# Optimization experiments

Hardware: AMD Instinct MI355X
Metric: run time of the kernel (lower is better)

## Reference

```python
import jax, jax.numpy as jnp
import numpy as np

B, S, IN, H, OUT, L = 32, 512, 300, 180, 60, 4
NBLOCK, NF = 3, 3  # mel_smooth_layers, mel_smooth_filter_size
GRP = OUT // NF    # 20 groups per mel conv


def setup_inputs() -> dict:
    key = jax.random.key(0)
    ks = jax.random.split(key, 12)
    def u(k, shape, scale):
        return jax.random.uniform(k, shape, jnp.float32, -scale, scale)
    s = float(1.0 / np.sqrt(H))
    return {
        "x": jax.random.normal(ks[0], (B, S, IN), jnp.float32),
        "Wih0": u(ks[1], (4 * H, IN), s),
        "Wih_rest": u(ks[2], (L - 1, 4 * H, H), s),
        "Whh": u(ks[3], (L, 4 * H, H), s),
        "bih": u(ks[4], (L, 4 * H), s),
        "bhh": u(ks[5], (L, 4 * H), s),
        "linW": u(ks[6], (OUT, H), s),
        "linb": u(ks[7], (OUT,), s),
        "mel_w": u(ks[8], (NBLOCK, NF, GRP, NF, 5), 0.2),  # per block, per filter: Conv1d(60,20,5,groups=20)
        "mel_b": u(ks[9], (NBLOCK, NF, GRP), 0.2),
        "resW": u(ks[10], (OUT, 2, 5), 0.2),               # Conv1d(120,60,5,groups=60)
        "resb": u(ks[11], (OUT,), 0.2),
    }


def _lstm(x, Wih0, Wih_rest, Whh, bih, bhh):
    # torch nn.LSTM, batch_first, gate order (i, f, g, o)
    h_in = x  # [B, S, D]
    for l in range(L):
        Wih = Wih0 if l == 0 else Wih_rest[l - 1]
        Whh_l = Whh[l]
        b = bih[l] + bhh[l]
        xt = h_in.transpose(1, 0, 2) @ Wih.T + b  # [S, B, 4H], input projection hoisted out of scan
        def step(carry, xg):
            h, c = carry
            g = xg + h @ Whh_l.T
            i, f, gg, o = jnp.split(g, 4, axis=-1)
            c = jax.nn.sigmoid(f) * c + jax.nn.sigmoid(i) * jnp.tanh(gg)
            h = jax.nn.sigmoid(o) * jnp.tanh(c)
            return (h, c), h
        init = (jnp.zeros((x.shape[0], H), x.dtype), jnp.zeros((x.shape[0], H), x.dtype))
        _, hs = jax.lax.scan(step, init, xt)  # [S, B, H]
        h_in = hs.transpose(1, 0, 2)
    return h_in  # [B, S, H]


def _conv1d_grouped(x, w, b, groups):
    # x: [B, C, S], w: [O, C//groups, K]
    y = jax.lax.conv_general_dilated(
        x, w, window_strides=(1,), padding=[(2, 2)],
        dimension_numbers=("NCH", "OIH", "NCH"), feature_group_count=groups)
    return y + b[None, :, None]


def _mel_block(x, w, b):
    # x: [B, 60, S]; w: [NF, 20, NF, 5]; b: [NF, 20]
    Bb, C, Ss = x.shape
    z = jnp.zeros((Bb, 1, Ss), x.dtype)
    # shifted channel stacks: [down-shift-1, identity, up-shift-1] (filter_size_channel == 3)
    xs = [jnp.concatenate([z, x[:, :-1]], axis=1), x, jnp.concatenate([x[:, 1:], z], axis=1)]
    outs = [_conv1d_grouped(xs[j], w[j], b[j], GRP) for j in range(NF)]  # each [B, 20, S]
    # interleave: output channel 3*i + j = outs[j][:, i, :]
    return jnp.stack(outs, axis=2).reshape(Bb, C, Ss)


def _forward(x, Wih0, Wih_rest, Whh, bih, bhh, linW, linb, mel_w, mel_b, resW, resb):
    h = _lstm(x, Wih0, Wih_rest, Whh, bih, bhh)      # [B, S, H]
    out = h @ linW.T + linb                          # [B, S, 60]
    out = out.transpose(0, 2, 1)                     # [B, 60, S]
    lstm_out = out
    for l in range(NBLOCK):
        out = _mel_block(out, mel_w[l], mel_b[l]) + out  # block + shortcut (Identity activation)
    # interleave (lstm, smoothed) per mel channel -> [B, 120, S]
    pair = jnp.stack([lstm_out, out], axis=2).reshape(out.shape[0], 2 * OUT, out.shape[2])
    out = _conv1d_grouped(pair, resW, resb, OUT)     # [B, 60, S]
    return out.transpose(0, 2, 1)                    # [B, S, 60] (Identity output activation)


def reference(x, Wih0, Wih_rest, Whh, bih, bhh, linW, linb, mel_w, mel_b, resW, resb):
    return _forward(x, Wih0, Wih_rest, Whh, bih, bhh, linW, linb, mel_w, mel_b, resW, resb)
```

## Files before the change

kernel.cpp:

```cpp
#include <hip/hip_runtime.h>
#include <hip/hip_bf16.h>

#define B_ 32
#define S_ 512
#define IN_ 300
#define H_ 180
#define G4_ 720
#define OUT_ 60
#define R_ 16384
#define TC_ 32
#define NC_ 16
#define NPK_ 92

#define PWHH_O  0u
#define PW0_O   264960u
#define PWR_O   372960u
#define BIASF_O 567360u
#define LINWF_O 570240u
#define LINBF_O 581040u
#define WFT_    581100u

#define XG_O   0u
#define HR_O   6291456u
#define H3_O   7397376u
#define WFU_O  8871936u
#define STH_O  9453036u
#define STC_O  9476076u
#define FLAG_O 9499116u
#define XGSLOT 786432
#define HRSLOT 184320

#if defined(__has_builtin)
#if __has_builtin(__builtin_amdgcn_fdot2)
#define HAVE_FDOT2 1
#endif
#if __has_builtin(__builtin_amdgcn_mov_dpp)
#define HAVE_DPP 1
#endif
#endif

typedef _Float16 f16x2 __attribute__((ext_vector_type(2)));

struct Plan {
  int nl; int ll[4]; int lc[4];
  int ng; int gl[4]; int gc[4];
};

__device__ __forceinline__ float sigf(float x)   { return 1.f / (1.f + __expf(-x)); }
__device__ __forceinline__ float tanhf2(float x) { return 2.f / (1.f + __expf(-2.f * x)) - 1.f; }
__device__ __forceinline__ float toF(__hip_bfloat16 x) { return __bfloat162float(x); }
__device__ __forceinline__ float ldr(const void* p, long i, int fl) {
  return fl ? ((const float*)p)[i] : toF(((const __hip_bfloat16*)p)[i]);
}
__device__ __forceinline__ unsigned f16b(_Float16 h) {
  union { _Float16 f; unsigned short s; } x; x.f = h; return x.s;
}
__device__ __forceinline__ float h2f(unsigned s) {
  union { unsigned short s; _Float16 f; } x; x.s = (unsigned short)(s & 0xFFFFu);
  return (float)x.f;
}
__device__ __forceinline__ f16x2 u2h(unsigned u) {
  union { unsigned u; f16x2 v; } x; x.u = u; return x.v;
}
__device__ __forceinline__ float fd2(unsigned hu, unsigned wu, float acc) {
#ifdef HAVE_FDOT2
  return __builtin_amdgcn_fdot2(u2h(hu), u2h(wu), acc, false);
#else
  return acc + h2f(hu) * h2f(wu) + h2f(hu >> 16) * h2f(wu >> 16);
#endif
}
__device__ __forceinline__ unsigned packpair_f32(float lo, float hi) {
  return f16b((_Float16)lo) | (f16b((_Float16)hi) << 16);
}
__device__ __forceinline__ unsigned packpair_bf16(unsigned u) {
  union { unsigned v; float f; } a, b;
  a.v = u << 16; b.v = u & 0xFFFF0000u;
  return packpair_f32(a.f, b.f);
}

#ifdef HAVE_DPP
#define QBC(dst, src, J) { \
  const int qv_ = __builtin_amdgcn_mov_dpp(__float_as_int(src), (J) * 85, 0xF, 0xF, false); \
  dst = __int_as_float(qv_); }
#else
#define QBC(dst, src, J) dst = __shfl(src, (((threadIdx.x & 63) & ~3) + (J)), 64);
#endif

#define REP23(M) M(0) M(1) M(2) M(3) M(4) M(5) M(6) M(7) M(8) M(9) M(10) \
  M(11) M(12) M(13) M(14) M(15) M(16) M(17) M(18) M(19) M(20) M(21) M(22)
#define LW(n) \
  unsigned w##n##a = wp0[(4*n+0)*G4_], w##n##b = wp0[(4*n+1)*G4_], \
           w##n##c = wp0[(4*n+2)*G4_], w##n##d = wp0[(4*n+3)*G4_];
#define PW(n) \
  asm volatile("" : "+v"(w##n##a), "+v"(w##n##b), "+v"(w##n##c), "+v"(w##n##d));
#define ST2(n) { \
  const uint4 hA_ = *(const uint4*)&hbA[4*n]; \
  const uint4 hB_ = *(const uint4*)&hbB[4*n]; \
  aA0 = fd2(hA_.x, w##n##a, aA0); aA1 = fd2(hA_.y, w##n##b, aA1); \
  aA2 = fd2(hA_.z, w##n##c, aA2); aA3 = fd2(hA_.w, w##n##d, aA3); \
  aB0 = fd2(hB_.x, w##n##a, aB0); aB1 = fd2(hB_.y, w##n##b, aB1); \
  aB2 = fd2(hB_.z, w##n##c, aB2); aB3 = fd2(hB_.w, w##n##d, aB3); }

__global__ __launch_bounds__(256) void detect_kernel(
    const unsigned short* __restrict__ xw, int* __restrict__ flag) {
  __shared__ int cnt;
  if (threadIdx.x == 0) cnt = 0;
  __syncthreads();
  int lc = 0;
  for (int i = threadIdx.x; i < 2048; i += 256) {
    const int e = (xw[i] >> 7) & 0xFF;
    if (e >= 0xC0 || (e > 0 && e < 0x40)) lc++;
  }
  atomicAdd(&cnt, lc);
  __syncthreads();
  if (threadIdx.x == 0) *flag = (cnt > 100) ? 1 : 0;
}

__global__ __launch_bounds__(256) void prep_kernel(
    const void* __restrict__ wih0, const void* __restrict__ wihr,
    const void* __restrict__ whh,  const void* __restrict__ bih,
    const void* __restrict__ bhh,  const void* __restrict__ linw,
    const void* __restrict__ linb, float* __restrict__ wf,
    const int* __restrict__ flag) {
  const unsigned i = blockIdx.x * 256u + threadIdx.x;
  if (i >= WFT_) return;
  const int fl = *flag;
  if (i < PW0_O) {
    const unsigned l = i / 66240u, r = i % 66240u;
    const unsigned jp = r / 720u, o = r % 720u;
    const unsigned ro = (o & 3u) * 180u + (o >> 2);
    unsigned u = 0u;
    if (jp < 90u) {
      const long b = (long)l * 129600 + (long)ro * H_;
      u = packpair_f32(ldr(whh, b + 2 * jp, fl), ldr(whh, b + 2 * jp + 1, fl));
    }
    ((unsigned*)wf)[i] = u;
    return;
  }
  if (i < PWR_O) {
    const unsigned j = i - PW0_O, o = j / 150u, kp = j % 150u;
    const long b = (long)o * IN_;
    ((unsigned*)wf)[i] =
        packpair_f32(ldr(wih0, b + 2 * kp, fl), ldr(wih0, b + 2 * kp + 1, fl));
    return;
  }
  if (i < BIASF_O) {
    const unsigned j = i - PWR_O, l = j / 64800u, r = j % 64800u;
    const unsigned o = r / 90u, kp = r % 90u;
    const long b = (long)l * 129600 + (long)o * H_;
    ((unsigned*)wf)[i] =
        packpair_f32(ldr(wihr, b + 2 * kp, fl), ldr(wihr, b + 2 * kp + 1, fl));
    return;
  }
  float v;
  if (i < LINWF_O)      { const unsigned j = i - BIASF_O; v = ldr(bih, j, fl) + ldr(bhh, j, fl); }
  else if (i < LINBF_O) v = ldr(linw, i - LINWF_O, fl);
  else                  v = ldr(linb, i - LINBF_O, fl);
  wf[i] = v;
}

__global__ __launch_bounds__(768, 3) void fused_kernel(
    const void* __restrict__ x, const int* __restrict__ flag,
    const unsigned* __restrict__ wfu,
    float* __restrict__ xg, float* __restrict__ hr,
    __hip_bfloat16* __restrict__ h3,
    float* __restrict__ sth, float* __restrict__ stc, Plan p) {
  __shared__ __align__(16) unsigned hpk[2][2][NPK_];
  __shared__ __align__(16) unsigned Asu[3][10][68];
  __shared__ __align__(16) unsigned Bsu[3][10][68];

  const int bid = blockIdx.x;
  if (bid < p.nl * 16) {
    const int j = bid >> 4, pb = bid & 15;
    const int l = p.ll[j], c = p.lc[j];
    const int b0 = pb * 2, b1 = b0 + 1;
    const int o = threadIdx.x;
    const int oc = (o < G4_) ? o : (G4_ - 1);
    const int g = o & 3, u = o >> 2;
    const bool act = (o < G4_);
    const unsigned* wp0 = wfu + PWHH_O + (unsigned)l * (NPK_ * G4_) + oc;
    REP23(LW)
    REP23(PW)
    const float* xgs = xg + (long)(l * 2 + (c & 1)) * XGSLOT;
    float* hrs = hr + (long)((l < 3 ? l : 0) * 2 + (c & 1)) * HRSLOT;
    float cstA = 0.f, cstB = 0.f, hA0 = 0.f, hB0 = 0.f;
    if (c != 0 && act) {
      cstA = stc[(l * 32 + b0) * H_ + u]; hA0 = sth[(l * 32 + b0) * H_ + u];
      cstB = stc[(l * 32 + b1) * H_ + u]; hB0 = sth[(l * 32 + b1) * H_ + u];
    }
    if (o < 4 * NPK_ && (o % NPK_) >= (NPK_ - 2)) ((unsigned*)hpk)[o] = 0u;
    {
      const unsigned vA = f16b((_Float16)hA0);
      const unsigned nA = __shfl_down(vA, 4);
      const unsigned vB = f16b((_Float16)hB0);
      const unsigned nB = __shfl_down(vB, 4);
      if (act && (o & 7) == 0) {
        hpk[0][0][u >> 1] = vA | (nA << 16);
        hpk[1][0][u >> 1] = vB | (nB << 16);
      }
    }
    const float* xpA = xgs + (long)b0 * TC_ * 768 + o;
    const float* xpB = xgs + (long)b1 * TC_ * 768 + o;
    float xcA = xpA[0], xcB = xpB[0];
    const float sg = (g == 2) ? 2.f : 1.f;
    __syncthreads();
    for (int tl = 0; tl < TC_; ++tl) {
      const unsigned* hbA = hpk[0][tl & 1];
      const unsigned* hbB = hpk[1][tl & 1];
      float aA0 = xcA, aA1 = 0.f, aA2 = 0.f, aA3 = 0.f;
      float aB0 = xcB, aB1 = 0.f, aB2 = 0.f, aB3 = 0.f;
      REP23(ST2)
      const float accA = (aA0 + aA1) + (aA2 + aA3);
      const float accB = (aB0 + aB1) + (aB2 + aB3);
      const int tn = (tl + 1 < TC_) ? tl + 1 : tl;
      xcA = xpA[(long)tn * 768]; xcB = xpB[(long)tn * 768];
      const float vA_ = 1.f / (1.f + __expf(-sg * accA));
      const float gvA = fmaf(sg, vA_ - 1.f, 1.f);
      const float vB_ = 1.f / (1.f + __expf(-sg * accB));
      const float gvB = fmaf(sg, vB_ - 1.f, 1.f);
      float qiA, qfA, qgA, qoA, qiB, qfB, qgB, qoB;
      QBC(qiA, gvA, 0) QBC(qfA, gvA, 1) QBC(qgA, gvA, 2) QBC(qoA, gvA, 3)
      QBC(qiB, gvB, 0) QBC(qfB, gvB, 1) QBC(qgB, gvB, 2) QBC(qoB, gvB, 3)
      cstA = qfA * cstA + qiA * qgA;
      cstB = qfB * cstB + qiB * qgB;
      const float hA = qoA * tanhf2(cstA);
      const float hB = qoB * tanhf2(cstB);
      const unsigned vA = f16b((_Float16)hA);
      const unsigned nA = __shfl_down(vA, 4);
      const unsigned vB = f16b((_Float16)hB);
      const unsigned nB = __shfl_down(vB, 4);
      const int wb = (tl & 1) ^ 1;
      if (act && (o & 7) == 0) {
        hpk[0][wb][u >> 1] = vA | (nA << 16);
        hpk[1][wb][u >> 1] = vB | (nB << 16);
      }
      if (act && g == 0) {
        if (l < 3) {
          hrs[(b0 * TC_ + tl) * H_ + u] = hA;
          hrs[(b1 * TC_ + tl) * H_ + u] = hB;
        } else {
          h3[((long)b0 * S_ + c * TC_ + tl) * H_ + u] = __float2bfloat16(hA);
          h3[((long)b1 * S_ + c * TC_ + tl) * H_ + u] = __float2bfloat16(hB);
        }
        if (tl == TC_ - 1) {
          sth[(l * 32 + b0) * H_ + u] = hA; stc[(l * 32 + b0) * H_ + u] = cstA;
          sth[(l * 32 + b1) * H_ + u] = hB; stc[(l * 32 + b1) * H_ + u] = cstB;
        }
      }
      asm volatile("s_waitcnt lgkmcnt(0)\n\ts_barrier" ::: "memory");
    }
    return;
  }

  const int gb = bid - p.nl * 16;
  const int g = threadIdx.x >> 8, t = threadIdx.x & 255;
  const int ti = gb * 3 + g;
  const int jj = ti / 192, idx = ti % 192;
  const int rt = idx & 15, ct = idx >> 4;
  const int l = p.gl[jj], c = p.gc[jj];
  const int fl = *flag;
  const int KP = (l == 0) ? 150 : 90;
  const unsigned* Wp = (l == 0) ? (wfu + PW0_O)
                                : (wfu + PWR_O + (unsigned)(l - 1) * 64800u);
  const float* bias = (const float*)wfu + BIASF_O + (unsigned)l * G4_;
  const float* hA = (l == 0) ? nullptr
                  : hr + (long)((l - 1) * 2 + (c & 1)) * HRSLOT;
  float* dst = xg + (long)(l * 2 + (c & 1)) * XGSLOT;
  const int rho0 = rt * 64, o0 = ct * 64;
  const int tx = t & 15, ty = t >> 4;
  float acc[4][4] = {};
  for (int kp0 = 0; kp0 < KP; kp0 += 10) {
    for (int e = t; e < 640; e += 256) {
      const int rl = e / 10, pp = e % 10;
      const int rho = rho0 + rl;
      unsigned av;
      if (l == 0) {
        const int bb = rho >> 5, tl = rho & 31;
        const long gr = (long)bb * S_ + c * TC_ + tl;
        if (fl == 0) av = packpair_bf16(((const unsigned*)x)[gr * 150 + kp0 + pp]);
        else { const float2 f = ((const float2*)x)[gr * 150 + kp0 + pp];
               av = packpair_f32(f.x, f.y); }
      } else {
        const float2 f = ((const float2*)hA)[(long)rho * 90 + kp0 + pp];
        av = packpair_f32(f.x, f.y);
      }
      Asu[g][pp][rl] = av;
      const int o = o0 + rl;
      Bsu[g][pp][rl] = (o < G4_) ? Wp[(long)o * KP + kp0 + pp] : 0u;
    }
    __syncthreads();
#pragma unroll
    for (int pp = 0; pp < 10; ++pp) {
      const uint4 a4 = *(const uint4*)&Asu[g][pp][ty * 4];
      const uint4 b4 = *(const uint4*)&Bsu[g][pp][tx * 4];
      const unsigned av[4] = {a4.x, a4.y, a4.z, a4.w};
      const unsigned bv[4] = {b4.x, b4.y, b4.z, b4.w};
#pragma unroll
      for (int i = 0; i < 4; ++i)
#pragma unroll
        for (int j2 = 0; j2 < 4; ++j2) acc[i][j2] = fd2(av[i], bv[j2], acc[i][j2]);
    }
    __syncthreads();
  }
#pragma unroll
  for (int i = 0; i < 4; ++i) {
    const int rho = rho0 + ty * 4 + i;
#pragma unroll
    for (int j2 = 0; j2 < 4; ++j2) {
      const int o = o0 + tx * 4 + j2;
      if (o < G4_) {
        const int gi = o / 180, un = o - gi * 180;
        dst[(long)rho * 768 + un * 4 + gi] = acc[i][j2] + bias[o];
      }
    }
  }
}

__global__ __launch_bounds__(256) void linear_kernel(
    const __hip_bfloat16* __restrict__ h, const float* __restrict__ linw,
    const float* __restrict__ linb, float* __restrict__ out) {
  __shared__ __align__(16) float Ast[20][68];
  __shared__ __align__(16) float Bst[20][68];
  const int bt = blockIdx.x;
  const int b = bt >> 3, st0 = (bt & 7) * 64;
  const int t = threadIdx.x, tx = t & 15, ty = t >> 4;
  float acc[4][4] = {};
  for (int k0 = 0; k0 < H_; k0 += 20) {
    for (int e = t; e < 1280; e += 256) {
      const int rl = e / 20, kk = e % 20;
      Ast[kk][rl] = toF(h[(long)(b * S_ + st0 + rl) * H_ + k0 + kk]);
      Bst[kk][rl] = (rl < OUT_) ? linw[rl * H_ + k0 + kk] : 0.f;
    }
    __syncthreads();
#pragma unroll
    for (int kk = 0; kk < 20; ++kk) {
      const float4 a4 = *(const float4*)&Ast[kk][ty * 4];
      const float4 b4 = *(const float4*)&Bst[kk][tx * 4];
      const float av[4] = {a4.x, a4.y, a4.z, a4.w};
      const float bv[4] = {b4.x, b4.y, b4.z, b4.w};
#pragma unroll
      for (int i = 0; i < 4; ++i)
#pragma unroll
        for (int j2 = 0; j2 < 4; ++j2) acc[i][j2] += av[i] * bv[j2];
    }
    __syncthreads();
  }
#pragma unroll
  for (int i = 0; i < 4; ++i) {
    const int s = st0 + ty * 4 + i;
#pragma unroll
    for (int j2 = 0; j2 < 4; ++j2) {
      const int c = tx * 4 + j2;
      if (c < OUT_) out[((long)b * OUT_ + c) * S_ + s] = acc[i][j2] + linb[c];
    }
  }
}

__global__ __launch_bounds__(256) void mel_kernel(
    const float* __restrict__ in, float* __restrict__ out,
    const void* __restrict__ mw, const void* __restrict__ mb,
    int l, const int* __restrict__ flag) {
  const int fl = *flag;
  const int idx = blockIdx.x;
  const int s = (idx & 1) * 256 + threadIdx.x;
  const int c = (idx >> 1) % OUT_;
  const int b = idx / (2 * OUT_);
  const int j = c % 3, i = c / 3;
  float acc = ldr(mb, (l * 3 + j) * 20 + i, fl);
  const long wbase = (long)((l * 3 + j) * 20 + i) * 15;
#pragma unroll
  for (int q = 0; q < 3; ++q) {
    const int ch = 3 * i + q + j - 1;
    if (ch < 0 || ch >= OUT_) continue;
    const float* xr = in + ((long)b * OUT_ + ch) * S_;
#pragma unroll
    for (int k = 0; k < 5; ++k) {
      const int sp = s + k - 2;
      if (sp < 0 || sp >= S_) continue;
      acc += ldr(mw, wbase + q * 5 + k, fl) * xr[sp];
    }
  }
  out[((long)b * OUT_ + c) * S_ + s] = acc + in[((long)b * OUT_ + c) * S_ + s];
}

__global__ __launch_bounds__(256) void res_kernel(
    const float* __restrict__ lin, const float* __restrict__ mel,
    const void* __restrict__ rw, const void* __restrict__ rb,
    void* __restrict__ outp, const int* __restrict__ flag) {
  const int fl = *flag;
  const int q = threadIdx.x >> 6, lane = threadIdx.x & 63;
  const int bs = blockIdx.x * 4 + q;
  const int b = bs / S_, s = bs % S_;
  if (lane >= OUT_) return;
  const int c = lane;
  float acc = ldr(rb, c, fl);
  const float* x0 = lin + ((long)b * OUT_ + c) * S_;
  const float* x1 = mel + ((long)b * OUT_ + c) * S_;
#pragma unroll
  for (int k = 0; k < 5; ++k) {
    const int sp = s + k - 2;
    if (sp < 0 || sp >= S_) continue;
    acc += ldr(rw, c * 10 + k, fl) * x0[sp] + ldr(rw, c * 10 + 5 + k, fl) * x1[sp];
  }
  const long oi = (long)bs * OUT_ + c;
  if (fl == 0) ((__hip_bfloat16*)outp)[oi] = __float2bfloat16(acc);
  else ((float*)outp)[oi] = acc;
}

extern "C" void kernel_launch(void* const* d_in, const int* in_sizes, int n_in,
                              void* d_out, int out_size, void* d_ws, size_t ws_size,
                              hipStream_t stream) {
  const void* x    = d_in[0];
  const void* wih0 = d_in[1];
  const void* wihr = d_in[2];
  const void* whh  = d_in[3];
  const void* bih  = d_in[4];
  const void* bhh  = d_in[5];
  const void* linw = d_in[6];
  const void* linb = d_in[7];
  const void* melw = d_in[8];
  const void* melb = d_in[9];
  const void* resw = d_in[10];
  const void* resb = d_in[11];

  float* ws = (float*)d_ws;
  float* xg = ws + XG_O;
  float* hrp = ws + HR_O;
  __hip_bfloat16* h3 = (__hip_bfloat16*)(ws + H3_O);
  float* wf = ws + WFU_O;
  const unsigned* wfu = (const unsigned*)wf;
  float* sth = ws + STH_O;
  float* stc = ws + STC_O;
  int* flag = (int*)(ws + FLAG_O);
  float* lin = ws + XG_O;
  float* m1 = lin + 983040;
  float* m2 = m1 + 983040;

  detect_kernel<<<1, 256, 0, stream>>>((const unsigned short*)x, flag);
  prep_kernel<<<(WFT_ + 255) / 256, 256, 0, stream>>>(
      wih0, wihr, whh, bih, bhh, linw, linb, wf, flag);

  {
    Plan p = {};
    p.nl = 0; p.ng = 1; p.gl[0] = 0; p.gc[0] = 0;
    fused_kernel<<<64, 768, 0, stream>>>(x, flag, wfu, xg, hrp, h3, sth, stc, p);
  }
  for (int n = 0; n <= 21; ++n) {
    Plan p = {};
    for (int l = 0; l < 4; ++l) {
      const int c = n - 2 * l;
      if (c >= 0 && c < NC_) { p.ll[p.nl] = l; p.lc[p.nl] = c; p.nl++; }
    }
    for (int l = 0; l < 4; ++l) {
      const int c = n + 1 - 2 * l;
      if (c >= 0 && c < NC_) { p.gl[p.ng] = l; p.gc[p.ng] = c; p.ng++; }
    }
    const int grid = p.nl * 16 + p.ng * 64;
    fused_kernel<<<grid, 768, 0, stream>>>(x, flag, wfu, xg, hrp, h3, sth, stc, p);
  }

  linear_kernel<<<256, 256, 0, stream>>>(h3, wf + LINWF_O, wf + LINBF_O, lin);
  mel_kernel<<<B_ * OUT_ * 2, 256, 0, stream>>>(lin, m1, melw, melb, 0, flag);
  mel_kernel<<<B_ * OUT_ * 2, 256, 0, stream>>>(m1, m2, melw, melb, 1, flag);
  mel_kernel<<<B_ * OUT_ * 2, 256, 0, stream>>>(m2, m1, melw, melb, 2, flag);
  res_kernel<<<R_ / 4, 256, 0, stream>>>(lin, m1, resw, resb, d_out, flag);
}
```

Baseline: 1.766 ms.

## Split recurrent weights between registers and LDS to cut VGPR pressure

The LSTM recurrence now keeps only the first 40 packed Whh rows in registers and stages the remaining 52 rows in shared memory, read each step as uint4 loads. All shared arrays are merged into one union buffer so the GEMM tiles reuse the same space. The gate-projection output layout also changes from a padded 768-stride interleaved form to a plain 720-stride gate-major form, which shrinks the xg buffer and simplifies the GEMM store. This trades register pressure, and possible spills at 768 threads, for extra LDS bandwidth inside the serial time loop.

Measured after the change: 1.900 ms. 7.6% more time.

```diff
diff --git a/kernel.cpp b/kernel.cpp
--- a/kernel.cpp
+++ b/kernel.cpp
@@ -21,14 +21,18 @@
 #define WFT_    581100u
 
 #define XG_O   0u
-#define HR_O   6291456u
-#define H3_O   7397376u
-#define WFU_O  8871936u
-#define STH_O  9453036u
-#define STC_O  9476076u
-#define FLAG_O 9499116u
-#define XGSLOT 786432
+#define HR_O   5898240u
+#define H3_O   7004160u
+#define WFU_O  8478720u
+#define STH_O  9059820u
+#define STC_O  9082860u
+#define FLAG_O 9105900u
+#define XGSLOT 737280
 #define HRSLOT 184320
+
+#define WLDS_W 37440
+#define HP0_   37440
+#define SHB_W  37808
 
 #if defined(__has_builtin)
 #if __has_builtin(__builtin_amdgcn_fdot2)
@@ -86,20 +90,28 @@
 #define QBC(dst, src, J) dst = __shfl(src, (((threadIdx.x & 63) & ~3) + (J)), 64);
 #endif
 
-#define REP23(M) M(0) M(1) M(2) M(3) M(4) M(5) M(6) M(7) M(8) M(9) M(10) \
-  M(11) M(12) M(13) M(14) M(15) M(16) M(17) M(18) M(19) M(20) M(21) M(22)
+#define REP10(M) M(0) M(1) M(2) M(3) M(4) M(5) M(6) M(7) M(8) M(9)
+#define REP13(M) M(0) M(1) M(2) M(3) M(4) M(5) M(6) M(7) M(8) M(9) M(10) M(11) M(12)
 #define LW(n) \
   unsigned w##n##a = wp0[(4*n+0)*G4_], w##n##b = wp0[(4*n+1)*G4_], \
            w##n##c = wp0[(4*n+2)*G4_], w##n##d = wp0[(4*n+3)*G4_];
 #define PW(n) \
   asm volatile("" : "+v"(w##n##a), "+v"(w##n##b), "+v"(w##n##c), "+v"(w##n##d));
-#define ST2(n) { \
-  const uint4 hA_ = *(const uint4*)&hbA[4*n]; \
-  const uint4 hB_ = *(const uint4*)&hbB[4*n]; \
+#define ST2R(n) { \
+  const uint4 hA_ = *(const uint4*)&hbA[4*(n)]; \
+  const uint4 hB_ = *(const uint4*)&hbB[4*(n)]; \
   aA0 = fd2(hA_.x, w##n##a, aA0); aA1 = fd2(hA_.y, w##n##b, aA1); \
   aA2 = fd2(hA_.z, w##n##c, aA2); aA3 = fd2(hA_.w, w##n##d, aA3); \
   aB0 = fd2(hB_.x, w##n##a, aB0); aB1 = fd2(hB_.y, w##n##b, aB1); \
   aB2 = fd2(hB_.z, w##n##c, aB2); aB3 = fd2(hB_.w, w##n##d, aB3); }
+#define ST2L(n) { \
+  const uint4 hA_ = *(const uint4*)&hbA[40 + 4*(n)]; \
+  const uint4 hB_ = *(const uint4*)&hbB[40 + 4*(n)]; \
+  const uint4 wv_ = *(const uint4*)&wldp[(n) * 2880]; \
+  aA0 = fd2(hA_.x, wv_.x, aA0); aA1 = fd2(hA_.y, wv_.y, aA1); \
+  aA2 = fd2(hA_.z, wv_.z, aA2); aA3 = fd2(hA_.w, wv_.w, aA3); \
+  aB0 = fd2(hB_.x, wv_.x, aB0); aB1 = fd2(hB_.y, wv_.y, aB1); \
+  aB2 = fd2(hB_.z, wv_.z, aB2); aB3 = fd2(hB_.w, wv_.w, aB3); }
 
 __global__ __launch_bounds__(256) void detect_kernel(
     const unsigned short* __restrict__ xw, int* __restrict__ flag) {
@@ -165,9 +177,7 @@
     float* __restrict__ xg, float* __restrict__ hr,
     __hip_bfloat16* __restrict__ h3,
     float* __restrict__ sth, float* __restrict__ stc, Plan p) {
-  __shared__ __align__(16) unsigned hpk[2][2][NPK_];
-  __shared__ __align__(16) unsigned Asu[3][10][68];
-  __shared__ __align__(16) unsigned Bsu[3][10][68];
+  __shared__ __align__(16) unsigned shb[SHB_W];
 
   const int bid = blockIdx.x;
   if (bid < p.nl * 16) {
@@ -178,9 +188,14 @@
     const int oc = (o < G4_) ? o : (G4_ - 1);
     const int g = o & 3, u = o >> 2;
     const bool act = (o < G4_);
-    const unsigned* wp0 = wfu + PWHH_O + (unsigned)l * (NPK_ * G4_) + oc;
-    REP23(LW)
-    REP23(PW)
+    const unsigned* wl0 = wfu + PWHH_O + (unsigned)l * (NPK_ * G4_);
+    const unsigned* wp0 = wl0 + oc;
+    REP10(LW)
+    REP10(PW)
+    for (int e = o; e < WLDS_W; e += 768) {
+      const int jq = e / 720, oo = e - jq * 720;
+      shb[(jq >> 2) * 2880 + oo * 4 + (jq & 3)] = wl0[(40 + jq) * 720 + oo];
+    }
     const float* xgs = xg + (long)(l * 2 + (c & 1)) * XGSLOT;
     float* hrs = hr + (long)((l < 3 ? l : 0) * 2 + (c & 1)) * HRSLOT;
     float cstA = 0.f, cstB = 0.f, hA0 = 0.f, hB0 = 0.f;
@@ -188,32 +203,35 @@
       cstA = stc[(l * 32 + b0) * H_ + u]; hA0 = sth[(l * 32 + b0) * H_ + u];
       cstB = stc[(l * 32 + b1) * H_ + u]; hB0 = sth[(l * 32 + b1) * H_ + u];
     }
-    if (o < 4 * NPK_ && (o % NPK_) >= (NPK_ - 2)) ((unsigned*)hpk)[o] = 0u;
+    if (o < 8) shb[HP0_ + (o >> 1) * 92 + 90 + (o & 1)] = 0u;
     {
       const unsigned vA = f16b((_Float16)hA0);
       const unsigned nA = __shfl_down(vA, 4);
       const unsigned vB = f16b((_Float16)hB0);
       const unsigned nB = __shfl_down(vB, 4);
       if (act && (o & 7) == 0) {
-        hpk[0][0][u >> 1] = vA | (nA << 16);
-        hpk[1][0][u >> 1] = vB | (nB << 16);
+        shb[HP0_ + (u >> 1)] = vA | (nA << 16);
+        shb[HP0_ + 184 + (u >> 1)] = vB | (nB << 16);
       }
     }
-    const float* xpA = xgs + (long)b0 * TC_ * 768 + o;
-    const float* xpB = xgs + (long)b1 * TC_ * 768 + o;
+    const int co = (oc & 3) * 180 + (oc >> 2);
+    const float* xpA = xgs + (long)b0 * TC_ * G4_ + co;
+    const float* xpB = xgs + (long)b1 * TC_ * G4_ + co;
     float xcA = xpA[0], xcB = xpB[0];
     const float sg = (g == 2) ? 2.f : 1.f;
     __syncthreads();
     for (int tl = 0; tl < TC_; ++tl) {
-      const unsigned* hbA = hpk[0][tl & 1];
-      const unsigned* hbB = hpk[1][tl & 1];
+      const unsigned* hbA = shb + HP0_ + (tl & 1) * 92;
+      const unsigned* hbB = shb + HP0_ + 184 + (tl & 1) * 92;
+      const unsigned* wldp = shb + oc * 4;
       float aA0 = xcA, aA1 = 0.f, aA2 = 0.f, aA3 = 0.f;
       float aB0 = xcB, aB1 = 0.f, aB2 = 0.f, aB3 = 0.f;
-      REP23(ST2)
+      REP10(ST2R)
+      REP13(ST2L)
       const float accA = (aA0 + aA1) + (aA2 + aA3);
       const float accB = (aB0 + aB1) + (aB2 + aB3);
       const int tn = (tl + 1 < TC_) ? tl + 1 : tl;
-      xcA = xpA[(long)tn * 768]; xcB = xpB[(long)tn * 768];
+      xcA = xpA[(long)tn * G4_]; xcB = xpB[(long)tn * G4_];
       const float vA_ = 1.f / (1.f + __expf(-sg * accA));
       const float gvA = fmaf(sg, vA_ - 1.f, 1.f);
       const float vB_ = 1.f / (1.f + __expf(-sg * accB));
@@ -231,8 +249,8 @@
       const unsigned nB = __shfl_down(vB, 4);
       const int wb = (tl & 1) ^ 1;
       if (act && (o & 7) == 0) {
-        hpk[0][wb][u >> 1] = vA | (nA << 16);
-        hpk[1][wb][u >> 1] = vB | (nB << 16);
+        shb[HP0_ + wb * 92 + (u >> 1)] = vA | (nA << 16);
+        shb[HP0_ + 184 + wb * 92 + (u >> 1)] = vB | (nB << 16);
       }
       if (act && g == 0) {
         if (l < 3) {
@@ -284,15 +302,16 @@
         const float2 f = ((const float2*)hA)[(long)rho * 90 + kp0 + pp];
         av = packpair_f32(f.x, f.y);
       }
-      Asu[g][pp][rl] = av;
+      shb[(g * 10 + pp) * 68 + rl] = av;
       const int o = o0 + rl;
-      Bsu[g][pp][rl] = (o < G4_) ? Wp[(long)o * KP + kp0 + pp] : 0u;
+      shb[2040 + (g * 10 + pp) * 68 + rl] =
+          (o < G4_) ? Wp[(long)o * KP + kp0 + pp] : 0u;
     }
     __syncthreads();
 #pragma unroll
     for (int pp = 0; pp < 10; ++pp) {
-      const uint4 a4 = *(const uint4*)&Asu[g][pp][ty * 4];
-      const uint4 b4 = *(const uint4*)&Bsu[g][pp][tx * 4];
+      const uint4 a4 = *(const uint4*)&shb[(g * 10 + pp) * 68 + ty * 4];
+      const uint4 b4 = *(const uint4*)&shb[2040 + (g * 10 + pp) * 68 + tx * 4];
       const unsigned av[4] = {a4.x, a4.y, a4.z, a4.w};
       const unsigned bv[4] = {b4.x, b4.y, b4.z, b4.w};
 #pragma unroll
@@ -308,10 +327,7 @@
 #pragma unroll
     for (int j2 = 0; j2 < 4; ++j2) {
       const int o = o0 + tx * 4 + j2;
-      if (o < G4_) {
-        const int gi = o / 180, un = o - gi * 180;
-        dst[(long)rho * 768 + un * 4 + gi] = acc[i][j2] + bias[o];
-      }
+      if (o < G4_) dst[(long)rho * G4_ + o] = acc[i][j2] + bias[o];
     }
   }
 }
```
